# Optimization experiments

Hardware: AMD Instinct MI355X
Metric: run time of the kernel (lower is better)

The kernel has to match this reference:

```python
import math
import jax, jax.numpy as jnp
import numpy as np


def _tokenformer_theta(scores):
    # L2-normalize along last dim, scale by sqrt(n), then exact GELU (torch F.gelu default)
    n = scores.shape[-1]
    l2 = jnp.maximum(jnp.linalg.norm(scores, ord=2, axis=-1, keepdims=True), 1e-8)
    scaled = scores * (math.sqrt(n) / l2)
    return jax.nn.gelu(scaled, approximate=False)


def setup_inputs() -> dict:
    key = jax.random.key(0)
    k1, k2, k3 = jax.random.split(key, 3)
    B, T, C = 4, 2048, 1024
    heads, num_tokens = 8, 1024
    key_hd, val_hd = C // heads, 1024 // heads
    x = jax.random.normal(k1, (B, T, C), dtype=jnp.float32)
    # kaiming_uniform_(a=sqrt(5)) on [heads, num_tokens, head_dim]: bound = sqrt(6/((1+5)*fan_in)) = 1/sqrt(fan_in)
    bk = 1.0 / math.sqrt(num_tokens)
    key_tokens = jax.random.uniform(k2, (heads, num_tokens, key_hd), minval=-bk, maxval=bk, dtype=jnp.float32)
    val_tokens = jax.random.uniform(k3, (heads, num_tokens, val_hd), minval=-bk, maxval=bk, dtype=jnp.float32)
    return {"x": x, "key_tokens": key_tokens, "val_tokens": val_tokens}


def reference(x, key_tokens, val_tokens):
    B, T, C = x.shape
    H, N, Dk = key_tokens.shape
    # q: [B, H, T, Dk]
    q = x.reshape(B, T, H, Dk).transpose(0, 2, 1, 3)
    # scores: [B, H, T, N]
    scores = jnp.einsum('bhtd,hnd->bhtn', q, key_tokens)
    scores = _tokenformer_theta(scores)
    # ThresHot: hard hot-mask keeping entries above the per-row mean (straight-through quantizer)
    mask = scores > jnp.mean(scores, axis=-1, keepdims=True)
    scores = jnp.where(mask, scores, 0.0)
    # out: [B, H, T, Dv] -> [B, T, H*Dv]
    out = jnp.einsum('bhtn,hnv->bhtv', scores, val_tokens)
    return out.transpose(0, 2, 1, 3).reshape(B, T, -1)
```

## Files before the change

kernel.cpp:

```cpp
#include <hip/hip_runtime.h>
#include <cstdint>
#include <cmath>


typedef __bf16 bf16x8 __attribute__((ext_vector_type(8)));
typedef float  f32x16 __attribute__((ext_vector_type(16)));
typedef unsigned short u16x8 __attribute__((ext_vector_type(8)));

__device__ __forceinline__ unsigned short bfbits(__bf16 b) {
  return __builtin_bit_cast(unsigned short, b);
}

__device__ __forceinline__ float gelu_s(float raw, float c707, float chalf) {
  const float s = raw * c707;
  const float a = fabsf(s);
  float u = fmaf(a, 4.30638e-5f, 2.765672e-4f);
  u = fmaf(u, a, 1.520143e-4f);
  u = fmaf(u, a, 9.2705272e-3f);
  u = fmaf(u, a, 4.22820123e-2f);
  u = fmaf(u, a, 7.05230784e-2f);
  u = fmaf(u, a, 1.0f);
  const float r  = __builtin_amdgcn_rcpf(u);
  const float r2 = r * r;
  const float r4 = r2 * r2;
  const float r8 = r4 * r4;
  const float r16 = r8 * r8;
  const float er = copysignf(1.0f - r16, s);
  const float hf = raw * chalf;
  return fmaf(hf, er, hf);
}

__global__ void prep_kv(const float* __restrict__ key,
                        const float* __restrict__ val,
                        unsigned short* __restrict__ kh,
                        unsigned short* __restrict__ kl,
                        unsigned short* __restrict__ vp) {
  const int gid = blockIdx.x * 256 + threadIdx.x;
  if (gid < 131072) {
    const int h  = gid >> 14;
    const int kc = (gid >> 10) & 15;
    const int n  = gid & 1023;
    const float* src = key + ((size_t)(h << 10) + n) * 128 + kc * 8;
    const float4 f0 = *(const float4*)src;
    const float4 f1 = *(const float4*)(src + 4);
    const float fv[8] = {f0.x, f0.y, f0.z, f0.w, f1.x, f1.y, f1.z, f1.w};
    u16x8 hv, lv;
#pragma unroll
    for (int e = 0; e < 8; ++e) {
      const __bf16 hb = (__bf16)fv[e];
      hv[e] = bfbits(hb);
      lv[e] = bfbits((__bf16)(fv[e] - (float)hb));
    }
    const size_t o = ((size_t)(h * 16 + kc) * 1024 + n) * 8;
    *(u16x8*)(kh + o) = hv;
    *(u16x8*)(kl + o) = lv;
  } else {
    const int tid = gid - 131072;
    const int h   = tid >> 14;
    const int s2  = (tid >> 7) & 127;
    const int v   = tid & 127;
    const float* src = val + ((size_t)(h << 10) + s2 * 8) * 128 + v;
    u16x8 ov;
#pragma unroll
    for (int e = 0; e < 8; ++e) ov[e] = bfbits((__bf16)src[(size_t)e * 128]);
    *(u16x8*)(vp + ((size_t)(h * 128 + s2) * 128 + v) * 8) = ov;
  }
}

#define RED1   131072
#define RED2   135168
#define SMEMSZ 139264

__global__ __launch_bounds__(1024, 4) void fused_mhk(
    const float* __restrict__ x,
    const unsigned short* __restrict__ k_hi,
    const unsigned short* __restrict__ k_lo,
    const unsigned short* __restrict__ v_pk,
    float* __restrict__ out)
{
  extern __shared__ char smem[];
  const int tid  = threadIdx.x;
  const int wave = tid >> 6;
  const int lane = tid & 63;
  const int l31  = lane & 31;
  const int hi   = lane >> 5;

  const int bid = blockIdx.x;
  const int h   = bid & 7;
  const int g8  = bid >> 3;
  const int b   = g8 & 3;
  const int tt  = g8 >> 2;
  const int t0  = tt * 64;

  {
    const float* xq = x + ((size_t)(b * 2048 + t0)) * 1024 + h * 128;
    const int r  = tid >> 4;
    const int kc = tid & 15;
    const float* sp = xq + (size_t)r * 1024 + kc * 8;
    const float4 f0 = *(const float4*)sp;
    const float4 f1 = *(const float4*)(sp + 4);
    const float fv[8] = {f0.x, f0.y, f0.z, f0.w, f1.x, f1.y, f1.z, f1.w};
    bf16x8 hv; u16x8 lv;
#pragma unroll
    for (int e = 0; e < 8; ++e) {
      const __bf16 hb = (__bf16)fv[e];
      hv[e] = hb;
      lv[e] = bfbits((__bf16)(fv[e] - (float)hb));
    }
    const int g = kc * 64 + (r ^ ((kc >> 1) & 7));
    *(bf16x8*)(smem + g * 16) = hv;
    *(u16x8*)(smem + 16384 + g * 16) = lv;
  }
  __syncthreads();

  f32x16 acc[2][2];
#pragma unroll
  for (int t = 0; t < 2; ++t)
#pragma unroll
    for (int qt = 0; qt < 2; ++qt)
#pragma unroll
      for (int i = 0; i < 16; ++i) acc[t][qt][i] = 0.f;

  {
    const unsigned short* kph = k_hi + (size_t)h * 131072;
    const unsigned short* kpl = k_lo + (size_t)h * 131072;
    const size_t kb = (size_t)hi * 8192 + (size_t)(wave * 64 + l31) * 8;
    const int hi64 = hi * 64;
#pragma unroll
    for (int s = 0; s < 8; ++s) {
      bf16x8 bqh[2], bql[2];
#pragma unroll
      for (int qt = 0; qt < 2; ++qt) {
        const int gx = (2 * s) * 64 + hi64 + ((qt * 32 + l31) ^ s);
        bqh[qt] = *(const bf16x8*)(smem + gx * 16);
        bql[qt] = *(const bf16x8*)(smem + 16384 + gx * 16);
      }
      const unsigned short* kah = kph + kb + s * 16384;
      const unsigned short* kal = kpl + kb + s * 16384;
#pragma unroll
      for (int t = 0; t < 2; ++t) {
        const bf16x8 ah = *(const bf16x8*)(kah + t * 256);
        const bf16x8 al = *(const bf16x8*)(kal + t * 256);
        acc[t][0] = __builtin_amdgcn_mfma_f32_32x32x16_bf16(ah, bqh[0], acc[t][0], 0, 0, 0);
        acc[t][1] = __builtin_amdgcn_mfma_f32_32x32x16_bf16(ah, bqh[1], acc[t][1], 0, 0, 0);
        acc[t][0] = __builtin_amdgcn_mfma_f32_32x32x16_bf16(ah, bql[0], acc[t][0], 0, 0, 0);
        acc[t][1] = __builtin_amdgcn_mfma_f32_32x32x16_bf16(ah, bql[1], acc[t][1], 0, 0, 0);
        acc[t][0] = __builtin_amdgcn_mfma_f32_32x32x16_bf16(al, bqh[0], acc[t][0], 0, 0, 0);
        acc[t][1] = __builtin_amdgcn_mfma_f32_32x32x16_bf16(al, bqh[1], acc[t][1], 0, 0, 0);
      }
    }
  }

  float* red1 = (float*)(smem + RED1);
  float* red2 = (float*)(smem + RED2);

  float ss0 = 0.f, ss1 = 0.f;
#pragma unroll
  for (int t = 0; t < 2; ++t)
#pragma unroll
    for (int i = 0; i < 16; ++i) {
      ss0 += acc[t][0][i] * acc[t][0][i];
      ss1 += acc[t][1][i] * acc[t][1][i];
    }
  ss0 += __shfl_xor(ss0, 32);
  ss1 += __shfl_xor(ss1, 32);
  red1[wave * 64 + lane] = hi ? ss1 : ss0;
  __syncthreads();
  float sum0 = 0.f, sum1 = 0.f;
#pragma unroll
  for (int w = 0; w < 16; ++w) {
    sum0 += red1[w * 64 + l31];
    sum1 += red1[w * 64 + 32 + l31];
  }
  const float scale0 = 32.0f / fmaxf(sqrtf(sum0), 1e-8f);
  const float scale1 = 32.0f / fmaxf(sqrtf(sum1), 1e-8f);
  const float c707_0 = scale0 * 0.70710678118654752f;
  const float c707_1 = scale1 * 0.70710678118654752f;
  const float chalf0 = scale0 * 0.5f;
  const float chalf1 = scale1 * 0.5f;

  float gs0 = 0.f, gs1 = 0.f;
#pragma unroll
  for (int t = 0; t < 2; ++t)
#pragma unroll
    for (int i = 0; i < 16; ++i) {
      const float g0 = gelu_s(acc[t][0][i], c707_0, chalf0);
      acc[t][0][i] = g0; gs0 += g0;
      const float g1 = gelu_s(acc[t][1][i], c707_1, chalf1);
      acc[t][1][i] = g1; gs1 += g1;
    }
  gs0 += __shfl_xor(gs0, 32);
  gs1 += __shfl_xor(gs1, 32);
  red2[wave * 64 + lane] = hi ? gs1 : gs0;
  __syncthreads();
  float mean0 = 0.f, mean1 = 0.f;
#pragma unroll
  for (int w = 0; w < 16; ++w) {
    mean0 += red2[w * 64 + l31];
    mean1 += red2[w * 64 + 32 + l31];
  }
  mean0 *= (1.0f / 1024.0f);
  mean1 *= (1.0f / 1024.0f);

#pragma unroll
  for (int t = 0; t < 2; ++t) {
#pragma unroll
    for (int qt = 0; qt < 2; ++qt) {
      const float mn = qt ? mean1 : mean0;
      const int q = qt * 32 + l31;
#pragma unroll
      for (int gi = 0; gi < 4; ++gi) {
        float g0 = acc[t][qt][4 * gi + 0]; g0 = (g0 > mn) ? g0 : 0.f;
        float g1 = acc[t][qt][4 * gi + 1]; g1 = (g1 > mn) ? g1 : 0.f;
        float g2 = acc[t][qt][4 * gi + 2]; g2 = (g2 > mn) ? g2 : 0.f;
        float g3 = acc[t][qt][4 * gi + 3]; g3 = (g3 > mn) ? g3 : 0.f;
        uint2 pk;
        pk.x = (unsigned)bfbits((__bf16)g0) | ((unsigned)bfbits((__bf16)g1) << 16);
        pk.y = (unsigned)bfbits((__bf16)g2) | ((unsigned)bfbits((__bf16)g3) << 16);
        const int ng = wave * 8 + t * 4 + gi;
        const int swz = (t * 4 + gi) & 7;
        *(uint2*)(smem + (ng * 64 + (q ^ swz)) * 16 + hi * 8) = pk;
      }
    }
  }
  __syncthreads();

  if (wave >= 8) return;
  const int qt2 = wave >> 2;
  const int vt  = wave & 3;
  const int q   = qt2 * 32 + l31;

  f32x16 o;
#pragma unroll
  for (int i = 0; i < 16; ++i) o[i] = 0.f;

  const unsigned short* vb = v_pk + (size_t)h * 131072 + (size_t)hi * 1024 +
                             (size_t)(vt * 32 + l31) * 8;
#pragma unroll 8
  for (int ks = 0; ks < 64; ++ks) {
    const int ng = 2 * ks + hi;
    const bf16x8 aa = *(const bf16x8*)(smem + (ng * 64 + (q ^ (ng & 7))) * 16);
    const bf16x8 bb = *(const bf16x8*)(vb + (size_t)ks * 2048);
    o = __builtin_amdgcn_mfma_f32_32x32x16_bf16(aa, bb, o, 0, 0, 0);
  }

  float* op = out + ((size_t)(b * 2048 + t0 + qt2 * 32)) * 1024 +
              h * 128 + vt * 32 + l31;
#pragma unroll
  for (int r = 0; r < 16; ++r) {
    const int qr = (r & 3) + 8 * (r >> 2) + 4 * hi;
    op[(size_t)qr * 1024] = o[r];
  }
}


extern "C" void kernel_launch(void* const* d_in, const int* in_sizes, int n_in,
                              void* d_out, int out_size, void* d_ws, size_t ws_size,
                              hipStream_t stream) {
  const float* x   = (const float*)d_in[0];
  const float* key = (const float*)d_in[1];
  const float* val = (const float*)d_in[2];
  float* out = (float*)d_out;

  if (ws_size < (size_t)6 * 1024 * 1024) return;

  unsigned short* k_hi = (unsigned short*)d_ws;
  unsigned short* k_lo = k_hi + 1048576;
  unsigned short* v_pk = k_lo + 1048576;

  prep_kv<<<dim3(1024), dim3(256), 0, stream>>>(key, val, k_hi, k_lo, v_pk);
  fused_mhk<<<dim3(1024), dim3(1024), SMEMSZ, stream>>>(x, k_hi, k_lo, v_pk, out);
}
```

Measured before the change: 113.6 us.

## Split PV GEMM across all 16 waves with split-K reduction and prefetch operands

The second GEMM (scores times value tokens) previously ran on only 8 of 16 waves. It is now split over all 16 waves: four groups each take a quarter of the token dimension and compute two 32-column tiles, and the partial results are reduced through shared memory. Key-token and value-token fragments are also software-prefetched one step ahead, and the first ones are loaded before the barriers, to hide global-load latency. This adds an extra LDS reduction pass, two more barriers and more register pressure.

Measured after the change: 164.4 us. +44.8%, slower.

```diff
diff --git a/kernel.cpp b/kernel.cpp
--- a/kernel.cpp
+++ b/kernel.cpp
@@ -111,6 +111,15 @@
     *(bf16x8*)(smem + g * 16) = hv;
     *(u16x8*)(smem + 16384 + g * 16) = lv;
   }
+
+  const unsigned short* kph = k_hi + (size_t)h * 131072;
+  const unsigned short* kpl = k_lo + (size_t)h * 131072;
+  const size_t kb = (size_t)hi * 8192 + (size_t)(wave * 64 + l31) * 8;
+  bf16x8 kch0 = *(const bf16x8*)(kph + kb);
+  bf16x8 kch1 = *(const bf16x8*)(kph + kb + 256);
+  bf16x8 kcl0 = *(const bf16x8*)(kpl + kb);
+  bf16x8 kcl1 = *(const bf16x8*)(kpl + kb + 256);
+
   __syncthreads();
 
   f32x16 acc[2][2];
@@ -122,32 +131,39 @@
       for (int i = 0; i < 16; ++i) acc[t][qt][i] = 0.f;
 
   {
-    const unsigned short* kph = k_hi + (size_t)h * 131072;
-    const unsigned short* kpl = k_lo + (size_t)h * 131072;
-    const size_t kb = (size_t)hi * 8192 + (size_t)(wave * 64 + l31) * 8;
     const int hi64 = hi * 64;
 #pragma unroll
     for (int s = 0; s < 8; ++s) {
-      bf16x8 bqh[2], bql[2];
-#pragma unroll
-      for (int qt = 0; qt < 2; ++qt) {
-        const int gx = (2 * s) * 64 + hi64 + ((qt * 32 + l31) ^ s);
-        bqh[qt] = *(const bf16x8*)(smem + gx * 16);
-        bql[qt] = *(const bf16x8*)(smem + 16384 + gx * 16);
+      bf16x8 knh0, knh1, knl0, knl1;
+      if (s < 7) {
+        const unsigned short* kah = kph + kb + (s + 1) * 16384;
+        const unsigned short* kal = kpl + kb + (s + 1) * 16384;
+        knh0 = *(const bf16x8*)(kah);
+        knh1 = *(const bf16x8*)(kah + 256);
+        knl0 = *(const bf16x8*)(kal);
+        knl1 = *(const bf16x8*)(kal + 256);
       }
-      const unsigned short* kah = kph + kb + s * 16384;
-      const unsigned short* kal = kpl + kb + s * 16384;
-#pragma unroll
-      for (int t = 0; t < 2; ++t) {
-        const bf16x8 ah = *(const bf16x8*)(kah + t * 256);
-        const bf16x8 al = *(const bf16x8*)(kal + t * 256);
-        acc[t][0] = __builtin_amdgcn_mfma_f32_32x32x16_bf16(ah, bqh[0], acc[t][0], 0, 0, 0);
-        acc[t][1] = __builtin_amdgcn_mfma_f32_32x32x16_bf16(ah, bqh[1], acc[t][1], 0, 0, 0);
-        acc[t][0] = __builtin_amdgcn_mfma_f32_32x32x16_bf16(ah, bql[0], acc[t][0], 0, 0, 0);
-        acc[t][1] = __builtin_amdgcn_mfma_f32_32x32x16_bf16(ah, bql[1], acc[t][1], 0, 0, 0);
-        acc[t][0] = __builtin_amdgcn_mfma_f32_32x32x16_bf16(al, bqh[0], acc[t][0], 0, 0, 0);
-        acc[t][1] = __builtin_amdgcn_mfma_f32_32x32x16_bf16(al, bqh[1], acc[t][1], 0, 0, 0);
-      }
+      const int gx0 = (2 * s) * 64 + hi64 + (l31 ^ s);
+      const int gx1 = (2 * s) * 64 + hi64 + ((32 + l31) ^ s);
+      const bf16x8 bqh0 = *(const bf16x8*)(smem + gx0 * 16);
+      const bf16x8 bql0 = *(const bf16x8*)(smem + 16384 + gx0 * 16);
+      const bf16x8 bqh1 = *(const bf16x8*)(smem + gx1 * 16);
+      const bf16x8 bql1 = *(const bf16x8*)(smem + 16384 + gx1 * 16);
+
+      acc[0][0] = __builtin_amdgcn_mfma_f32_32x32x16_bf16(kch0, bqh0, acc[0][0], 0, 0, 0);
+      acc[0][1] = __builtin_amdgcn_mfma_f32_32x32x16_bf16(kch0, bqh1, acc[0][1], 0, 0, 0);
+      acc[0][0] = __builtin_amdgcn_mfma_f32_32x32x16_bf16(kch0, bql0, acc[0][0], 0, 0, 0);
+      acc[0][1] = __builtin_amdgcn_mfma_f32_32x32x16_bf16(kch0, bql1, acc[0][1], 0, 0, 0);
+      acc[0][0] = __builtin_amdgcn_mfma_f32_32x32x16_bf16(kcl0, bqh0, acc[0][0], 0, 0, 0);
+      acc[0][1] = __builtin_amdgcn_mfma_f32_32x32x16_bf16(kcl0, bqh1, acc[0][1], 0, 0, 0);
+      acc[1][0] = __builtin_amdgcn_mfma_f32_32x32x16_bf16(kch1, bqh0, acc[1][0], 0, 0, 0);
+      acc[1][1] = __builtin_amdgcn_mfma_f32_32x32x16_bf16(kch1, bqh1, acc[1][1], 0, 0, 0);
+      acc[1][0] = __builtin_amdgcn_mfma_f32_32x32x16_bf16(kch1, bql0, acc[1][0], 0, 0, 0);
+      acc[1][1] = __builtin_amdgcn_mfma_f32_32x32x16_bf16(kch1, bql1, acc[1][1], 0, 0, 0);
+      acc[1][0] = __builtin_amdgcn_mfma_f32_32x32x16_bf16(kcl1, bqh0, acc[1][0], 0, 0, 0);
+      acc[1][1] = __builtin_amdgcn_mfma_f32_32x32x16_bf16(kcl1, bqh1, acc[1][1], 0, 0, 0);
+
+      if (s < 7) { kch0 = knh0; kch1 = knh1; kcl0 = knl0; kcl1 = knl1; }
     }
   }
 
@@ -201,6 +217,16 @@
   }
   mean0 *= (1.0f / 1024.0f);
   mean1 *= (1.0f / 1024.0f);
+
+  const int qt2 = wave & 1;
+  const int vt2 = (wave >> 1) & 1;
+  const int nh  = wave >> 2;
+  const unsigned short* vbase = v_pk + (size_t)h * 131072;
+  const int vc0 = (vt2 * 64 + l31) * 8;
+
+  const int ng00 = nh * 32 + hi;
+  bf16x8 v0 = *(const bf16x8*)(vbase + (size_t)ng00 * 1024 + vc0);
+  bf16x8 v1 = *(const bf16x8*)(vbase + (size_t)ng00 * 1024 + vc0 + 256);
 
 #pragma unroll
   for (int t = 0; t < 2; ++t) {
@@ -225,31 +251,63 @@
   }
   __syncthreads();
 
-  if (wave >= 8) return;
-  const int qt2 = wave >> 2;
-  const int vt  = wave & 3;
-  const int q   = qt2 * 32 + l31;
-
-  f32x16 o;
-#pragma unroll
-  for (int i = 0; i < 16; ++i) o[i] = 0.f;
-
-  const unsigned short* vb = v_pk + (size_t)h * 131072 + (size_t)hi * 1024 +
-                             (size_t)(vt * 32 + l31) * 8;
-#pragma unroll 8
-  for (int ks = 0; ks < 64; ++ks) {
-    const int ng = 2 * ks + hi;
-    const bf16x8 aa = *(const bf16x8*)(smem + (ng * 64 + (q ^ (ng & 7))) * 16);
-    const bf16x8 bb = *(const bf16x8*)(vb + (size_t)ks * 2048);
-    o = __builtin_amdgcn_mfma_f32_32x32x16_bf16(aa, bb, o, 0, 0, 0);
+  f32x16 o0, o1;
+#pragma unroll
+  for (int i = 0; i < 16; ++i) { o0[i] = 0.f; o1[i] = 0.f; }
+
+  const int qrow = qt2 * 32 + l31;
+#pragma unroll
+  for (int ks = 0; ks < 16; ++ks) {
+    const int ng = nh * 32 + ks * 2 + hi;
+    const bf16x8 aa = *(const bf16x8*)(smem + (ng * 64 + (qrow ^ (ng & 7))) * 16);
+    bf16x8 p0, p1;
+    if (ks < 15) {
+      p0 = *(const bf16x8*)(vbase + (size_t)(ng + 2) * 1024 + vc0);
+      p1 = *(const bf16x8*)(vbase + (size_t)(ng + 2) * 1024 + vc0 + 256);
+    }
+    o0 = __builtin_amdgcn_mfma_f32_32x32x16_bf16(aa, v0, o0, 0, 0, 0);
+    o1 = __builtin_amdgcn_mfma_f32_32x32x16_bf16(aa, v1, o1, 0, 0, 0);
+    if (ks < 15) { v0 = p0; v1 = p1; }
+  }
+  __syncthreads();
+
+  if (nh != 0) {
+    const int bb = nh * 32768 + (wave & 3) * 8192 + lane * 128;
+#pragma unroll
+    for (int c = 0; c < 8; ++c) {
+      const int cc = ((c + lane) & 7) * 16;
+      float4 ch;
+      if (c < 4) ch = make_float4(o0[4*c], o0[4*c+1], o0[4*c+2], o0[4*c+3]);
+      else       ch = make_float4(o1[4*(c-4)], o1[4*(c-4)+1], o1[4*(c-4)+2], o1[4*(c-4)+3]);
+      *(float4*)(smem + bb + cc) = ch;
+    }
+  }
+  __syncthreads();
+  if (nh != 0) return;
+
+#pragma unroll
+  for (int src = 1; src < 4; ++src) {
+    const int bb = src * 32768 + (wave & 3) * 8192 + lane * 128;
+#pragma unroll
+    for (int c = 0; c < 8; ++c) {
+      const int cc = ((c + lane) & 7) * 16;
+      const float4 ch = *(const float4*)(smem + bb + cc);
+      if (c < 4) {
+        o0[4*c] += ch.x; o0[4*c+1] += ch.y; o0[4*c+2] += ch.z; o0[4*c+3] += ch.w;
+      } else {
+        o1[4*(c-4)] += ch.x; o1[4*(c-4)+1] += ch.y;
+        o1[4*(c-4)+2] += ch.z; o1[4*(c-4)+3] += ch.w;
+      }
+    }
   }
 
   float* op = out + ((size_t)(b * 2048 + t0 + qt2 * 32)) * 1024 +
-              h * 128 + vt * 32 + l31;
+              h * 128 + vt2 * 64 + l31;
 #pragma unroll
   for (int r = 0; r < 16; ++r) {
     const int qr = (r & 3) + 8 * (r >> 2) + 4 * hi;
-    op[(size_t)qr * 1024] = o[r];
+    op[(size_t)qr * 1024]      = o0[r];
+    op[(size_t)qr * 1024 + 32] = o1[r];
   }
 }
 
```

## Software-pipeline score and PV stages across four 64-row tiles per block

Applied to the files above, without the earlier changes.

Each block now handles four consecutive 64-row tiles, so there are 256 blocks instead of 1024. The score GEMM and GELU of tile i+1 overlap with the PV GEMM of tile i, which all 16 waves now share through 16x16x32 MFMAs. The x low-residual is stored as scaled fp8 in shared memory and expanded back to bf16, cutting LDS use. Partial outputs are accumulated with atomicAdd into a zero-filled output, which adds a memset and atomic traffic and gives up the x-row parallelism of the smaller blocks.

New measurement: 358.3 us. +215.5%, slower.

```diff
diff --git a/kernel.cpp b/kernel.cpp
--- a/kernel.cpp
+++ b/kernel.cpp
@@ -5,10 +5,80 @@
 
 typedef __bf16 bf16x8 __attribute__((ext_vector_type(8)));
 typedef float  f32x16 __attribute__((ext_vector_type(16)));
+typedef float  f32x4  __attribute__((ext_vector_type(4)));
 typedef unsigned short u16x8 __attribute__((ext_vector_type(8)));
+
+#if defined(__has_builtin)
+#if __has_builtin(__builtin_amdgcn_cvt_pk_f32_fp8) && __has_builtin(__builtin_amdgcn_cvt_pk_fp8_f32)
+#define HW_FP8 1
+#endif
+#endif
+#ifndef HW_FP8
+#define HW_FP8 0
+#endif
 
 __device__ __forceinline__ unsigned short bfbits(__bf16 b) {
   return __builtin_bit_cast(unsigned short, b);
+}
+
+__device__ __forceinline__ unsigned int enc_fp8_1(float f) {
+  unsigned int u = __float_as_uint(f);
+  unsigned int s = u >> 31;
+  u &= 0x7FFFFFFFu;
+  unsigned int r = (u + 0x7FFFFu + ((u >> 20) & 1u)) >> 20;
+  unsigned int mag = (r >= 968u) ? (r - 960u) : 0u;
+  if (mag > 127u) mag = 127u;
+  return (s << 7) | mag;
+}
+
+template <bool WORD>
+__device__ __forceinline__ unsigned int pack_fp8_pair(float a, float b,
+                                                      unsigned int old) {
+#if HW_FP8
+  return (unsigned int)__builtin_amdgcn_cvt_pk_fp8_f32(a, b, (int)old, WORD);
+#else
+  const unsigned int pk = enc_fp8_1(a) | (enc_fp8_1(b) << 8);
+  return WORD ? ((old & 0x0000FFFFu) | (pk << 16))
+              : ((old & 0xFFFF0000u) | pk);
+#endif
+}
+
+__device__ __forceinline__ unsigned short dec_fp8_1(unsigned int b) {
+  const unsigned int t = b & 0x7Fu;
+  unsigned int v = (t << 4) + 14080u;
+  v |= (b & 0x80u) << 8;
+  return (t >= 16u) ? (unsigned short)v : (unsigned short)0;
+}
+
+__device__ __forceinline__ bf16x8 dec_qlo(uint2 lo) {
+#if HW_FP8
+  const float S = 1.0f / 1024.0f;
+  auto p0 = __builtin_amdgcn_cvt_pk_f32_fp8((int)lo.x, false);
+  auto p1 = __builtin_amdgcn_cvt_pk_f32_fp8((int)lo.x, true);
+  auto p2 = __builtin_amdgcn_cvt_pk_f32_fp8((int)lo.y, false);
+  auto p3 = __builtin_amdgcn_cvt_pk_f32_fp8((int)lo.y, true);
+  unsigned int w0, w1, w2, w3;
+  asm("v_cvt_pk_bf16_f32 %0, %1, %2" : "=v"(w0) : "v"(p0[0] * S), "v"(p0[1] * S));
+  asm("v_cvt_pk_bf16_f32 %0, %1, %2" : "=v"(w1) : "v"(p1[0] * S), "v"(p1[1] * S));
+  asm("v_cvt_pk_bf16_f32 %0, %1, %2" : "=v"(w2) : "v"(p2[0] * S), "v"(p2[1] * S));
+  asm("v_cvt_pk_bf16_f32 %0, %1, %2" : "=v"(w3) : "v"(p3[0] * S), "v"(p3[1] * S));
+  uint4 uu = make_uint4(w0, w1, w2, w3);
+  return __builtin_bit_cast(bf16x8, uu);
+#else
+  unsigned short r0 = dec_fp8_1(lo.x & 0xFFu);
+  unsigned short r1 = dec_fp8_1((lo.x >> 8) & 0xFFu);
+  unsigned short r2 = dec_fp8_1((lo.x >> 16) & 0xFFu);
+  unsigned short r3 = dec_fp8_1(lo.x >> 24);
+  unsigned short r4 = dec_fp8_1(lo.y & 0xFFu);
+  unsigned short r5 = dec_fp8_1((lo.y >> 8) & 0xFFu);
+  unsigned short r6 = dec_fp8_1((lo.y >> 16) & 0xFFu);
+  unsigned short r7 = dec_fp8_1(lo.y >> 24);
+  uint4 uu = make_uint4((unsigned)r0 | ((unsigned)r1 << 16),
+                        (unsigned)r2 | ((unsigned)r3 << 16),
+                        (unsigned)r4 | ((unsigned)r5 << 16),
+                        (unsigned)r6 | ((unsigned)r7 << 16));
+  return __builtin_bit_cast(bf16x8, uu);
+#endif
 }
 
 __device__ __forceinline__ float gelu_s(float raw, float c707, float chalf) {
@@ -24,8 +94,7 @@
   const float r2 = r * r;
   const float r4 = r2 * r2;
   const float r8 = r4 * r4;
-  const float r16 = r8 * r8;
-  const float er = copysignf(1.0f - r16, s);
+  const float er = copysignf(1.0f - r8 * r8, s);
   const float hf = raw * chalf;
   return fmaf(hf, er, hf);
 }
@@ -67,9 +136,10 @@
   }
 }
 
-#define RED1   131072
-#define RED2   135168
-#define SMEMSZ 139264
+#define QHI_OFF 131072
+#define QLO_OFF 147456
+#define RED_OFF 155648
+#define SMEMSZ  159744
 
 __global__ __launch_bounds__(1024, 4) void fused_mhk(
     const float* __restrict__ x,
@@ -84,172 +154,231 @@
   const int lane = tid & 63;
   const int l31  = lane & 31;
   const int hi   = lane >> 5;
+  const int l15  = lane & 15;
+  const int l4   = lane >> 4;
 
   const int bid = blockIdx.x;
   const int h   = bid & 7;
-  const int g8  = bid >> 3;
-  const int b   = g8 & 3;
-  const int tt  = g8 >> 2;
-  const int t0  = tt * 64;
+  const int chunk = bid >> 3;
+  const int b   = chunk >> 3;
+  const int t0base = (chunk & 7) * 256;
+
+  const unsigned short* kph = k_hi + (size_t)h * 131072;
+  const unsigned short* kpl = k_lo + (size_t)h * 131072;
+  const unsigned short* vph = v_pk + (size_t)h * 131072;
+  float* red = (float*)(smem + RED_OFF);
+
+  const int pc = wave & 7;
+  const int pn = wave >> 3;
 
   {
-    const float* xq = x + ((size_t)(b * 2048 + t0)) * 1024 + h * 128;
-    const int r  = tid >> 4;
-    const int kc = tid & 15;
+    const float* xq = x + ((size_t)(b * 2048 + t0base)) * 1024 + h * 128;
+    const int r = tid >> 4, kc = tid & 15;
     const float* sp = xq + (size_t)r * 1024 + kc * 8;
     const float4 f0 = *(const float4*)sp;
     const float4 f1 = *(const float4*)(sp + 4);
     const float fv[8] = {f0.x, f0.y, f0.z, f0.w, f1.x, f1.y, f1.z, f1.w};
-    bf16x8 hv; u16x8 lv;
+    bf16x8 hv; float lv[8];
 #pragma unroll
     for (int e = 0; e < 8; ++e) {
       const __bf16 hb = (__bf16)fv[e];
       hv[e] = hb;
-      lv[e] = bfbits((__bf16)(fv[e] - (float)hb));
+      lv[e] = (fv[e] - (float)hb) * 1024.0f;
     }
     const int g = kc * 64 + (r ^ ((kc >> 1) & 7));
-    *(bf16x8*)(smem + g * 16) = hv;
-    *(u16x8*)(smem + 16384 + g * 16) = lv;
+    *(bf16x8*)(smem + QHI_OFF + g * 16) = hv;
+    unsigned int w0 = pack_fp8_pair<false>(lv[0], lv[1], 0u);
+    w0 = pack_fp8_pair<true>(lv[2], lv[3], w0);
+    unsigned int w1 = pack_fp8_pair<false>(lv[4], lv[5], 0u);
+    w1 = pack_fp8_pair<true>(lv[6], lv[7], w1);
+    *(uint2*)(smem + QLO_OFF + g * 8) = make_uint2(w0, w1);
   }
   __syncthreads();
 
   f32x16 acc[2][2];
-#pragma unroll
-  for (int t = 0; t < 2; ++t)
-#pragma unroll
-    for (int qt = 0; qt < 2; ++qt)
-#pragma unroll
-      for (int i = 0; i < 16; ++i) acc[t][qt][i] = 0.f;
-
-  {
-    const unsigned short* kph = k_hi + (size_t)h * 131072;
-    const unsigned short* kpl = k_lo + (size_t)h * 131072;
+  f32x4 pv[4];
+  float gs0 = 0.f, gs1 = 0.f;
+
+  for (int i = 0; i <= 4; ++i) {
+    const bool hasP = (i < 4);
+    const bool hasC = (i >= 1);
+
+    if (hasP) {
+#pragma unroll
+      for (int t = 0; t < 2; ++t)
+#pragma unroll
+        for (int qt = 0; qt < 2; ++qt)
+#pragma unroll
+          for (int e = 0; e < 16; ++e) acc[t][qt][e] = 0.f;
+    }
+    if (hasC) {
+#pragma unroll
+      for (int qs = 0; qs < 4; ++qs)
+#pragma unroll
+        for (int j = 0; j < 4; ++j) pv[qs][j] = 0.f;
+    }
+
     const size_t kb = (size_t)hi * 8192 + (size_t)(wave * 64 + l31) * 8;
-    const int hi64 = hi * 64;
-#pragma unroll
-    for (int s = 0; s < 8; ++s) {
-      bf16x8 bqh[2], bql[2];
-#pragma unroll
-      for (int qt = 0; qt < 2; ++qt) {
-        const int gx = (2 * s) * 64 + hi64 + ((qt * 32 + l31) ^ s);
-        bqh[qt] = *(const bf16x8*)(smem + gx * 16);
-        bql[qt] = *(const bf16x8*)(smem + 16384 + gx * 16);
-      }
-      const unsigned short* kah = kph + kb + s * 16384;
-      const unsigned short* kal = kpl + kb + s * 16384;
+#pragma unroll
+    for (int u = 0; u < 8; ++u) {
+      if (hasP) {
+        const int s = u;
+        bf16x8 bqh[2], bql[2];
+#pragma unroll
+        for (int qt = 0; qt < 2; ++qt) {
+          const int gx = (2 * s + hi) * 64 + ((qt * 32 + l31) ^ s);
+          bqh[qt] = *(const bf16x8*)(smem + QHI_OFF + gx * 16);
+          bql[qt] = dec_qlo(*(const uint2*)(smem + QLO_OFF + gx * 8));
+        }
+        const unsigned short* kah = kph + kb + s * 16384;
+        const unsigned short* kal = kpl + kb + s * 16384;
+#pragma unroll
+        for (int t = 0; t < 2; ++t) {
+          const bf16x8 ah = *(const bf16x8*)(kah + t * 256);
+          const bf16x8 al = *(const bf16x8*)(kal + t * 256);
+          acc[t][0] = __builtin_amdgcn_mfma_f32_32x32x16_bf16(ah, bqh[0], acc[t][0], 0, 0, 0);
+          acc[t][1] = __builtin_amdgcn_mfma_f32_32x32x16_bf16(ah, bqh[1], acc[t][1], 0, 0, 0);
+          acc[t][0] = __builtin_amdgcn_mfma_f32_32x32x16_bf16(ah, bql[0], acc[t][0], 0, 0, 0);
+          acc[t][1] = __builtin_amdgcn_mfma_f32_32x32x16_bf16(ah, bql[1], acc[t][1], 0, 0, 0);
+          acc[t][0] = __builtin_amdgcn_mfma_f32_32x32x16_bf16(al, bqh[0], acc[t][0], 0, 0, 0);
+          acc[t][1] = __builtin_amdgcn_mfma_f32_32x32x16_bf16(al, bqh[1], acc[t][1], 0, 0, 0);
+        }
+      }
+      if (hasC) {
+        const int s2 = pn * 64 + u * 4 + l4;
+        const bf16x8 bb = *(const bf16x8*)(vph + ((size_t)s2 * 128 + pc * 16 + l15) * 8);
+        const char* arow = smem + (size_t)s2 * 1024;
+#pragma unroll
+        for (int qs = 0; qs < 4; ++qs) {
+          const int q = qs * 16 + l15;
+          const bf16x8 aa = *(const bf16x8*)(arow + (q ^ (s2 & 7)) * 16);
+          pv[qs] = __builtin_amdgcn_mfma_f32_16x16x32_bf16(aa, bb, pv[qs], 0, 0, 0);
+        }
+      }
+    }
+    if (hasP) {
+      float ss0 = 0.f, ss1 = 0.f;
+#pragma unroll
+      for (int t = 0; t < 2; ++t)
+#pragma unroll
+        for (int e = 0; e < 16; ++e) {
+          ss0 += acc[t][0][e] * acc[t][0][e];
+          ss1 += acc[t][1][e] * acc[t][1][e];
+        }
+      ss0 += __shfl_xor(ss0, 32);
+      ss1 += __shfl_xor(ss1, 32);
+      red[wave * 64 + lane] = hi ? ss1 : ss0;
+    }
+    __syncthreads();
+
+    if (hasP) {
+      float sum0 = 0.f, sum1 = 0.f;
+#pragma unroll
+      for (int w = 0; w < 16; ++w) {
+        sum0 += red[w * 64 + l31];
+        sum1 += red[w * 64 + 32 + l31];
+      }
+      const float scale0 = 32.0f / fmaxf(sqrtf(sum0), 1e-8f);
+      const float scale1 = 32.0f / fmaxf(sqrtf(sum1), 1e-8f);
+      const float c707_0 = scale0 * 0.70710678118654752f;
+      const float c707_1 = scale1 * 0.70710678118654752f;
+      const float chalf0 = scale0 * 0.5f;
+      const float chalf1 = scale1 * 0.5f;
+      gs0 = 0.f; gs1 = 0.f;
+#pragma unroll
+      for (int t = 0; t < 2; ++t)
+#pragma unroll
+        for (int e = 0; e < 16; ++e) {
+          const float g0 = gelu_s(acc[t][0][e], c707_0, chalf0);
+          acc[t][0][e] = g0; gs0 += g0;
+          const float g1 = gelu_s(acc[t][1][e], c707_1, chalf1);
+          acc[t][1][e] = g1; gs1 += g1;
+        }
+      gs0 += __shfl_xor(gs0, 32);
+      gs1 += __shfl_xor(gs1, 32);
+    }
+    if (hasC) {
+#pragma unroll
+      for (int u = 8; u < 16; ++u) {
+        const int s2 = pn * 64 + u * 4 + l4;
+        const bf16x8 bb = *(const bf16x8*)(vph + ((size_t)s2 * 128 + pc * 16 + l15) * 8);
+        const char* arow = smem + (size_t)s2 * 1024;
+#pragma unroll
+        for (int qs = 0; qs < 4; ++qs) {
+          const int q = qs * 16 + l15;
+          const bf16x8 aa = *(const bf16x8*)(arow + (q ^ (s2 & 7)) * 16);
+          pv[qs] = __builtin_amdgcn_mfma_f32_16x16x32_bf16(aa, bb, pv[qs], 0, 0, 0);
+        }
+      }
+    }
+    if (i + 1 < 4) {
+      const float* xq = x + ((size_t)(b * 2048 + t0base + (i + 1) * 64)) * 1024 + h * 128;
+      const int r = tid >> 4, kc = tid & 15;
+      const float* sp = xq + (size_t)r * 1024 + kc * 8;
+      const float4 f0 = *(const float4*)sp;
+      const float4 f1 = *(const float4*)(sp + 4);
+      const float fv[8] = {f0.x, f0.y, f0.z, f0.w, f1.x, f1.y, f1.z, f1.w};
+      bf16x8 hv; float lv[8];
+#pragma unroll
+      for (int e = 0; e < 8; ++e) {
+        const __bf16 hb = (__bf16)fv[e];
+        hv[e] = hb;
+        lv[e] = (fv[e] - (float)hb) * 1024.0f;
+      }
+      const int g = kc * 64 + (r ^ ((kc >> 1) & 7));
+      *(bf16x8*)(smem + QHI_OFF + g * 16) = hv;
+      unsigned int w0 = pack_fp8_pair<false>(lv[0], lv[1], 0u);
+      w0 = pack_fp8_pair<true>(lv[2], lv[3], w0);
+      unsigned int w1 = pack_fp8_pair<false>(lv[4], lv[5], 0u);
+      w1 = pack_fp8_pair<true>(lv[6], lv[7], w1);
+      *(uint2*)(smem + QLO_OFF + g * 8) = make_uint2(w0, w1);
+    }
+    __syncthreads();
+
+    if (hasP) red[wave * 64 + lane] = hi ? gs1 : gs0;
+    if (hasC) {
+      const int t0c = t0base + (i - 1) * 64;
+      float* ob = out + ((size_t)(b * 2048 + t0c)) * 1024 + h * 128 + pc * 16 + l15;
+#pragma unroll
+      for (int qs = 0; qs < 4; ++qs)
+#pragma unroll
+        for (int j = 0; j < 4; ++j)
+          atomicAdd(ob + (size_t)(qs * 16 + l4 * 4 + j) * 1024, pv[qs][j]);
+    }
+    __syncthreads();
+
+    if (hasP) {
+      float mean0 = 0.f, mean1 = 0.f;
+#pragma unroll
+      for (int w = 0; w < 16; ++w) {
+        mean0 += red[w * 64 + l31];
+        mean1 += red[w * 64 + 32 + l31];
+      }
+      mean0 *= (1.0f / 1024.0f);
+      mean1 *= (1.0f / 1024.0f);
 #pragma unroll
       for (int t = 0; t < 2; ++t) {
-        const bf16x8 ah = *(const bf16x8*)(kah + t * 256);
-        const bf16x8 al = *(const bf16x8*)(kal + t * 256);
-        acc[t][0] = __builtin_amdgcn_mfma_f32_32x32x16_bf16(ah, bqh[0], acc[t][0], 0, 0, 0);
-        acc[t][1] = __builtin_amdgcn_mfma_f32_32x32x16_bf16(ah, bqh[1], acc[t][1], 0, 0, 0);
-        acc[t][0] = __builtin_amdgcn_mfma_f32_32x32x16_bf16(ah, bql[0], acc[t][0], 0, 0, 0);
-        acc[t][1] = __builtin_amdgcn_mfma_f32_32x32x16_bf16(ah, bql[1], acc[t][1], 0, 0, 0);
-        acc[t][0] = __builtin_amdgcn_mfma_f32_32x32x16_bf16(al, bqh[0], acc[t][0], 0, 0, 0);
-        acc[t][1] = __builtin_amdgcn_mfma_f32_32x32x16_bf16(al, bqh[1], acc[t][1], 0, 0, 0);
-      }
-    }
-  }
-
-  float* red1 = (float*)(smem + RED1);
-  float* red2 = (float*)(smem + RED2);
-
-  float ss0 = 0.f, ss1 = 0.f;
-#pragma unroll
-  for (int t = 0; t < 2; ++t)
-#pragma unroll
-    for (int i = 0; i < 16; ++i) {
-      ss0 += acc[t][0][i] * acc[t][0][i];
-      ss1 += acc[t][1][i] * acc[t][1][i];
-    }
-  ss0 += __shfl_xor(ss0, 32);
-  ss1 += __shfl_xor(ss1, 32);
-  red1[wave * 64 + lane] = hi ? ss1 : ss0;
-  __syncthreads();
-  float sum0 = 0.f, sum1 = 0.f;
-#pragma unroll
-  for (int w = 0; w < 16; ++w) {
-    sum0 += red1[w * 64 + l31];
-    sum1 += red1[w * 64 + 32 + l31];
-  }
-  const float scale0 = 32.0f / fmaxf(sqrtf(sum0), 1e-8f);
-  const float scale1 = 32.0f / fmaxf(sqrtf(sum1), 1e-8f);
-  const float c707_0 = scale0 * 0.70710678118654752f;
-  const float c707_1 = scale1 * 0.70710678118654752f;
-  const float chalf0 = scale0 * 0.5f;
-  const float chalf1 = scale1 * 0.5f;
-
-  float gs0 = 0.f, gs1 = 0.f;
-#pragma unroll
-  for (int t = 0; t < 2; ++t)
-#pragma unroll
-    for (int i = 0; i < 16; ++i) {
-      const float g0 = gelu_s(acc[t][0][i], c707_0, chalf0);
-      acc[t][0][i] = g0; gs0 += g0;
-      const float g1 = gelu_s(acc[t][1][i], c707_1, chalf1);
-      acc[t][1][i] = g1; gs1 += g1;
-    }
-  gs0 += __shfl_xor(gs0, 32);
-  gs1 += __shfl_xor(gs1, 32);
-  red2[wave * 64 + lane] = hi ? gs1 : gs0;
-  __syncthreads();
-  float mean0 = 0.f, mean1 = 0.f;
-#pragma unroll
-  for (int w = 0; w < 16; ++w) {
-    mean0 += red2[w * 64 + l31];
-    mean1 += red2[w * 64 + 32 + l31];
-  }
-  mean0 *= (1.0f / 1024.0f);
-  mean1 *= (1.0f / 1024.0f);
-
-#pragma unroll
-  for (int t = 0; t < 2; ++t) {
-#pragma unroll
-    for (int qt = 0; qt < 2; ++qt) {
-      const float mn = qt ? mean1 : mean0;
-      const int q = qt * 32 + l31;
-#pragma unroll
-      for (int gi = 0; gi < 4; ++gi) {
-        float g0 = acc[t][qt][4 * gi + 0]; g0 = (g0 > mn) ? g0 : 0.f;
-        float g1 = acc[t][qt][4 * gi + 1]; g1 = (g1 > mn) ? g1 : 0.f;
-        float g2 = acc[t][qt][4 * gi + 2]; g2 = (g2 > mn) ? g2 : 0.f;
-        float g3 = acc[t][qt][4 * gi + 3]; g3 = (g3 > mn) ? g3 : 0.f;
-        uint2 pk;
-        pk.x = (unsigned)bfbits((__bf16)g0) | ((unsigned)bfbits((__bf16)g1) << 16);
-        pk.y = (unsigned)bfbits((__bf16)g2) | ((unsigned)bfbits((__bf16)g3) << 16);
-        const int ng = wave * 8 + t * 4 + gi;
-        const int swz = (t * 4 + gi) & 7;
-        *(uint2*)(smem + (ng * 64 + (q ^ swz)) * 16 + hi * 8) = pk;
-      }
-    }
-  }
-  __syncthreads();
-
-  if (wave >= 8) return;
-  const int qt2 = wave >> 2;
-  const int vt  = wave & 3;
-  const int q   = qt2 * 32 + l31;
-
-  f32x16 o;
-#pragma unroll
-  for (int i = 0; i < 16; ++i) o[i] = 0.f;
-
-  const unsigned short* vb = v_pk + (size_t)h * 131072 + (size_t)hi * 1024 +
-                             (size_t)(vt * 32 + l31) * 8;
-#pragma unroll 8
-  for (int ks = 0; ks < 64; ++ks) {
-    const int ng = 2 * ks + hi;
-    const bf16x8 aa = *(const bf16x8*)(smem + (ng * 64 + (q ^ (ng & 7))) * 16);
-    const bf16x8 bb = *(const bf16x8*)(vb + (size_t)ks * 2048);
-    o = __builtin_amdgcn_mfma_f32_32x32x16_bf16(aa, bb, o, 0, 0, 0);
-  }
-
-  float* op = out + ((size_t)(b * 2048 + t0 + qt2 * 32)) * 1024 +
-              h * 128 + vt * 32 + l31;
-#pragma unroll
-  for (int r = 0; r < 16; ++r) {
-    const int qr = (r & 3) + 8 * (r >> 2) + 4 * hi;
-    op[(size_t)qr * 1024] = o[r];
+#pragma unroll
+        for (int qt = 0; qt < 2; ++qt) {
+          const float mn = qt ? mean1 : mean0;
+          const int q = qt * 32 + l31;
+#pragma unroll
+          for (int gi = 0; gi < 4; ++gi) {
+            float g0 = acc[t][qt][4 * gi + 0]; g0 = (g0 > mn) ? g0 : 0.f;
+            float g1 = acc[t][qt][4 * gi + 1]; g1 = (g1 > mn) ? g1 : 0.f;
+            float g2 = acc[t][qt][4 * gi + 2]; g2 = (g2 > mn) ? g2 : 0.f;
+            float g3 = acc[t][qt][4 * gi + 3]; g3 = (g3 > mn) ? g3 : 0.f;
+            uint2 pk;
+            pk.x = (unsigned)bfbits((__bf16)g0) | ((unsigned)bfbits((__bf16)g1) << 16);
+            pk.y = (unsigned)bfbits((__bf16)g2) | ((unsigned)bfbits((__bf16)g3) << 16);
+            const int ng = wave * 8 + t * 4 + gi;
+            const int swz = (t * 4 + gi) & 7;
+            *(uint2*)(smem + (ng * 64 + (q ^ swz)) * 16 + hi * 8) = pk;
+          }
+        }
+      }
+    }
+    __syncthreads();
   }
 }
 
@@ -268,6 +397,7 @@
   unsigned short* k_lo = k_hi + 1048576;
   unsigned short* v_pk = k_lo + 1048576;
 
+  (void)hipMemsetAsync(d_out, 0, (size_t)out_size * sizeof(float), stream);
   prep_kv<<<dim3(1024), dim3(256), 0, stream>>>(key, val, k_hi, k_lo, v_pk);
-  fused_mhk<<<dim3(1024), dim3(1024), SMEMSZ, stream>>>(x, k_hi, k_lo, v_pk, out);
-}
+  fused_mhk<<<dim3(256), dim3(1024), SMEMSZ, stream>>>(x, k_hi, k_lo, v_pk, out);
+}
```
